# Kernel tuning notes

Measured on AMD Instinct MI355X. Metric: run time of the kernel, lower is better.

Reference implementation:

```python
import jax, jax.numpy as jnp
import numpy as np

B, L, LC, C, CTX, H = 4, 2048, 512, 1024, 1024, 16
D = C // H
EPS = 1e-6
SCALE = 1.0 / np.float32(np.sqrt(D))


def _ln(x):
    # LayerNorm32, elementwise_affine applied outside when present
    mu = jnp.mean(x, axis=-1, keepdims=True)
    var = jnp.var(x, axis=-1, keepdims=True)
    return (x - mu) * jax.lax.rsqrt(var + EPS)


def _attn(q, k, v):
    # q: [B,Lq,H,D], k/v: [B,Lk,H,D] -> [B,Lq,C]
    s = jnp.einsum('bqhd,bkhd->bhqk', q, k) * SCALE
    p = jax.nn.softmax(s, axis=-1)
    o = jnp.einsum('bhqk,bkhd->bqhd', p, v)
    return o.reshape(o.shape[0], o.shape[1], C)


def setup_inputs() -> dict:
    key = jax.random.key(0)
    ks = jax.random.split(key, 12)
    s = 0.02
    w = lambda k, shape: (jax.random.normal(k, shape, jnp.float32) * s)
    z = lambda n: jnp.zeros((n,), jnp.float32)
    return {
        'x': jax.random.normal(ks[0], (B, L, C), jnp.float32),
        'mod': jax.random.normal(ks[1], (B, C), jnp.float32),
        'context': jax.random.normal(ks[2], (B, LC, CTX), jnp.float32),
        'w_ada': w(ks[3], (C, 6 * C)), 'b_ada': z(6 * C),
        'w_qkv': w(ks[4], (C, 3 * C)), 'b_qkv': z(3 * C),
        'w_so': w(ks[5], (C, C)), 'b_so': z(C),
        'g_n2': jnp.ones((C,), jnp.float32), 'b_n2': z(C),
        'w_cq': w(ks[6], (C, C)), 'b_cq': z(C),
        'w_ckv': w(ks[7], (CTX, 2 * C)), 'b_ckv': z(2 * C),
        'w_co': w(ks[8], (C, C)), 'b_co': z(C),
        'w_m1': w(ks[9], (C, 4 * C)), 'b_m1': z(4 * C),
        'w_m2': w(ks[10], (4 * C, C)), 'b_m2': z(C),
    }


def reference(x, mod, context, w_ada, b_ada, w_qkv, b_qkv, w_so, b_so,
              g_n2, b_n2, w_cq, b_cq, w_ckv, b_ckv, w_co, b_co,
              w_m1, b_m1, w_m2, b_m2):
    # adaLN modulation: SiLU -> Linear(C, 6C) -> chunk(6)
    ada = jax.nn.silu(mod) @ w_ada + b_ada  # [B, 6C]
    sh_msa, sc_msa, g_msa, sh_mlp, sc_mlp, g_mlp = jnp.split(ada, 6, axis=-1)
    ex = lambda t: t[:, None, :]  # broadcast per-sample over its token run

    # --- MSA branch ---
    h = _ln(x) * (1.0 + ex(sc_msa)) + ex(sh_msa)
    qkv = (h @ w_qkv + b_qkv).reshape(B, L, 3, H, D)
    h = _attn(qkv[:, :, 0], qkv[:, :, 1], qkv[:, :, 2]) @ w_so + b_so
    x = x + h * ex(g_msa)

    # --- MCA branch (norm2 has affine) ---
    h = _ln(x) * g_n2 + b_n2
    q = (h @ w_cq + b_cq).reshape(B, L, H, D)
    kv = (context @ w_ckv + b_ckv).reshape(B, LC, 2, H, D)
    h = _attn(q, kv[:, :, 0], kv[:, :, 1]) @ w_co + b_co
    x = x + h

    # --- FFN branch ---
    h = _ln(x) * (1.0 + ex(sc_mlp)) + ex(sh_mlp)
    h = jax.nn.gelu(h @ w_m1 + b_m1, approximate=False) @ w_m2 + b_m2
    x = x + h * ex(g_mlp)
    return x
```

## Files before the change

### kernel.cpp

```cpp
#include <hip/hip_runtime.h>
#include <cstdint>

typedef __bf16 bf16;
typedef __bf16 bf16x8 __attribute__((ext_vector_type(8)));
typedef __bf16 bf16x4 __attribute__((ext_vector_type(4)));
typedef float  floatx4 __attribute__((ext_vector_type(4)));
typedef unsigned int uint32x4 __attribute__((ext_vector_type(4)));

#define B_  4
#define L_  2048
#define LC_ 512
#define C_  1024
#define H_  16
#define D_  64

typedef const __attribute__((address_space(1))) unsigned int* as1_u32p;
typedef __attribute__((address_space(3))) unsigned int* as3_u32p;

__device__ __forceinline__ void async16(const void* g, void* l) {
  __builtin_amdgcn_global_load_lds((as1_u32p)g, (as3_u32p)l, 16, 0, 0);
}

__device__ __forceinline__ floatx4 mfma16(bf16x8 a, bf16x8 b, floatx4 c) {
  return __builtin_amdgcn_mfma_f32_16x16x32_bf16(a, b, c, 0, 0, 0);
}

__device__ __forceinline__ bool dt_bf16(const unsigned* dt) { return dt[0] == 0x3F803F80u; }

__device__ __forceinline__ float rd(const void* p, size_t i, bool bf) {
  return bf ? (float)((const bf16*)p)[i] : ((const float*)p)[i];
}

__global__ __launch_bounds__(256) void k_cvt(const void* __restrict__ src, bf16* __restrict__ dst,
                                             int N, const unsigned* __restrict__ dt) {
  bool bf = dt_bf16(dt);
  int i = (blockIdx.x * 256 + threadIdx.x) * 4;
  if (i + 3 < N) {
    for (int j = 0; j < 4; ++j) dst[i + j] = (bf16)rd(src, i + j, bf);
  } else {
    for (int j = 0; j < 4 && i + j < N; ++j) dst[i + j] = (bf16)rd(src, i + j, bf);
  }
}

struct CvtSrcs { const void* s[9]; };
__global__ __launch_bounds__(256) void k_cvt_all(CvtSrcs c, bf16* __restrict__ dst,
                                                 const unsigned* __restrict__ dt) {
  bool bf = dt_bf16(dt);
  int i = blockIdx.x * 256 + threadIdx.x;
  if (i >= 15360) return;
  const int pre[10] = {0, 3072, 4096, 5120, 6144, 7168, 9216, 10240, 14336, 15360};
  int seg = 0;
  #pragma unroll
  for (int k = 1; k < 9; ++k) if (i >= pre[k]) seg = k;
  dst[i] = (bf16)rd(c.s[seg], i - pre[seg], bf);
}

__global__ __launch_bounds__(256) void k_silu(const void* __restrict__ mod, float* __restrict__ sm,
                                              const unsigned* __restrict__ dt) {
  bool bf = dt_bf16(dt);
  int i = blockIdx.x * 256 + threadIdx.x;
  if (i < B_ * C_) {
    float v = rd(mod, i, bf);
    sm[i] = v / (1.f + __expf(-v));
  }
}

__global__ __launch_bounds__(256) void k_ada(const float* __restrict__ sm, const void* __restrict__ w,
                                             float* __restrict__ part, const unsigned* __restrict__ dt) {
  bool bf = dt_bf16(dt);
  int idx = blockIdx.x * 256 + threadIdx.x;
  int b = idx / 6144, j = idx - b * 6144;
  int k0 = blockIdx.y * 256;
  const float* s = sm + b * C_;
  float acc = 0.f;
  if (bf) {
    const bf16* W = (const bf16*)w;
    for (int k = k0; k < k0 + 256; ++k) acc += s[k] * (float)W[(size_t)k * 6144 + j];
  } else {
    const float* W = (const float*)w;
    for (int k = k0; k < k0 + 256; ++k) acc += s[k] * W[(size_t)k * 6144 + j];
  }
  part[(size_t)blockIdx.y * 24576 + idx] = acc;
}

__global__ __launch_bounds__(256) void k_ada_red(const float* __restrict__ part, const void* __restrict__ bv,
                                                 float* __restrict__ ada, const unsigned* __restrict__ dt) {
  bool bf = dt_bf16(dt);
  int idx = blockIdx.x * 256 + threadIdx.x;
  int j = idx % 6144;
  ada[idx] = rd(bv, j, bf) + part[idx] + part[24576 + idx] + part[49152 + idx] + part[73728 + idx];
}

struct TransDesc { const void* src; bf16* dst; int R, Cc, nCb, pre; };
struct TransDescs { TransDesc d[7]; };
__global__ __launch_bounds__(256) void k_trans_all(TransDescs t, const unsigned* __restrict__ dt) {
  bool bf = dt_bf16(dt);
  __shared__ bf16 tile[32][33];
  int blk = blockIdx.x;
  int di = 0;
  #pragma unroll
  for (int i = 1; i < 7; ++i) if (blk >= t.d[i].pre) di = i;
  const void* src = t.d[di].src;
  bf16* dst = t.d[di].dst;
  int R = t.d[di].R, Cc = t.d[di].Cc;
  int local = blk - t.d[di].pre;
  int bx = local % t.d[di].nCb, by = local / t.d[di].nCb;
  int c0 = bx * 32, r0 = by * 32;
  int tx = threadIdx.x & 31, ty = threadIdx.x >> 5;
  for (int i = 0; i < 4; ++i)
    tile[ty * 4 + i][tx] = (bf16)rd(src, (size_t)(r0 + ty * 4 + i) * Cc + c0 + tx, bf);
  __syncthreads();
  for (int i = 0; i < 4; ++i)
    dst[(size_t)(c0 + ty * 4 + i) * R + r0 + tx] = tile[tx][ty * 4 + i];
}

__global__ __launch_bounds__(256) void k_vt(const bf16* __restrict__ src, int ld, int off, int Lk,
                                            bf16* __restrict__ VT) {
  __shared__ bf16 tile[32][33];
  int l0 = blockIdx.x * 32;
  int d0 = blockIdx.y * 32;
  int bh = blockIdx.z, b = bh >> 4, h = bh & 15;
  int tx = threadIdx.x & 31, ty = threadIdx.x >> 5;
  for (int i = 0; i < 4; ++i) {
    int l = l0 + ty * 4 + i;
    tile[ty * 4 + i][tx] = src[((size_t)b * Lk + l) * ld + off + h * 64 + d0 + tx];
  }
  __syncthreads();
  for (int i = 0; i < 4; ++i) {
    int d = d0 + ty * 4 + i;
    VT[((size_t)bh * 64 + d) * Lk + l0 + tx] = tile[tx][ty * 4 + i];
  }
}

__global__ __launch_bounds__(256) void k_ln(const void* __restrict__ xraw, const float* __restrict__ xf,
                                            const unsigned* __restrict__ dt, bf16* __restrict__ out,
                                            const float* __restrict__ ada, int scOff, int shOff, float scAdd,
                                            const bf16* __restrict__ gcol, const bf16* __restrict__ bcol) {
  int row = blockIdx.x;
  int b = row >> 11;
  int base = row * C_ + threadIdx.x * 4;
  float v[4];
  if (xf) {
    for (int i = 0; i < 4; ++i) v[i] = xf[base + i];
  } else {
    bool bf = dt_bf16(dt);
    for (int i = 0; i < 4; ++i) v[i] = rd(xraw, base + i, bf);
  }
  float s1 = 0.f, s2 = 0.f;
  for (int i = 0; i < 4; ++i) { s1 += v[i]; s2 += v[i] * v[i]; }
  for (int m = 1; m < 64; m <<= 1) { s1 += __shfl_xor(s1, m); s2 += __shfl_xor(s2, m); }
  __shared__ float r1[4], r2[4];
  int w = threadIdx.x >> 6;
  if ((threadIdx.x & 63) == 0) { r1[w] = s1; r2[w] = s2; }
  __syncthreads();
  s1 = r1[0] + r1[1] + r1[2] + r1[3];
  s2 = r2[0] + r2[1] + r2[2] + r2[3];
  float mu = s1 * (1.f / (float)C_);
  float var = fmaxf(s2 * (1.f / (float)C_) - mu * mu, 0.f);
  float rstd = rsqrtf(var + 1e-6f);
  for (int i = 0; i < 4; ++i) {
    int c = threadIdx.x * 4 + i;
    float sc, sh;
    if (ada) { sc = scAdd + ada[b * 6144 + scOff + c]; sh = ada[b * 6144 + shOff + c]; }
    else     { sc = (float)gcol[c];                    sh = (float)bcol[c]; }
    out[base + i] = (bf16)((v[i] - mu) * rstd * sc + sh);
  }
}

template <int MODE>
__global__ __launch_bounds__(256) void k_gemm(const bf16* __restrict__ A, const bf16* __restrict__ Bt,
                                              const bf16* __restrict__ bias, void* __restrict__ outv,
                                              int M, int N, int K,
                                              const void* __restrict__ resid,
                                              const float* __restrict__ ada, int gateOff,
                                              const unsigned* __restrict__ dt,
                                              float qs, int qN) {
  __shared__ bf16 As[2 * 8192];
  __shared__ bf16 Bs[2 * 8192];
  const int tid = threadIdx.x;
  const int w = tid >> 6, lane = tid & 63;
  const int wr = w & 1, wc = w >> 1;
  const int g = lane >> 4, t = lane & 15;

  const int nbx = gridDim.x;
  const int nwg = nbx * gridDim.y;
  const int orig = blockIdx.y * nbx + blockIdx.x;
  const int qq = nwg >> 3, rrm = nwg & 7;
  const int xcd = orig & 7, sidx = orig >> 3;
  const int wgid = (xcd < rrm ? xcd * (qq + 1) : rrm * (qq + 1) + (xcd - rrm) * qq) + sidx;
  const int rowA0 = (wgid / nbx) * 128, rowB0 = (wgid % nbx) * 128;

  const int scol = ((lane & 3) ^ ((lane >> 3) & 3)) * 8;
  const bf16* Ag = A  + (size_t)(rowA0 + w * 32 + (lane >> 2)) * K + scol;
  const bf16* Bg = Bt + (size_t)(rowB0 + w * 32 + (lane >> 2)) * K + scol;

  auto stage = [&](int kb, int bufsel) {
    bf16* Ad = As + bufsel * 8192 + w * 1024;
    bf16* Bd = Bs + bufsel * 8192 + w * 1024;
    async16(Ag + kb,                       Ad);
    async16(Ag + kb + (size_t)16 * K,      Ad + 512);
    async16(Ag + kb + 32,                  Ad + 4096);
    async16(Ag + kb + 32 + (size_t)16 * K, Ad + 4096 + 512);
    async16(Bg + kb,                       Bd);
    async16(Bg + kb + (size_t)16 * K,      Bd + 512);
    async16(Bg + kb + 32,                  Bd + 4096);
    async16(Bg + kb + 32 + (size_t)16 * K, Bd + 4096 + 512);
  };

  floatx4 acc[4][4];
  for (int i = 0; i < 4; ++i) for (int j = 0; j < 4; ++j) for (int r = 0; r < 4; ++r) acc[i][j][r] = 0.f;

  stage(0, 0);
  __syncthreads();

  const int rsw = (t >> 1) & 3;

  const int nkb = K >> 6;
  for (int it = 0; it < nkb; ++it) {
    const int cur = it & 1;
    if (it + 1 < nkb) stage((it + 1) << 6, cur ^ 1);
    const bf16* Asb = As + cur * 8192;
    const bf16* Bsb = Bs + cur * 8192;
    __builtin_amdgcn_s_setprio(1);
    #pragma unroll
    for (int kk = 0; kk < 2; ++kk) {
      const int gc = (g ^ rsw) * 8;
      bf16x8 af[4], bfr[4];
      #pragma unroll
      for (int mt = 0; mt < 4; ++mt) af[mt]  = *(const bf16x8*)&Asb[kk * 4096 + (wr * 64 + mt * 16 + t) * 32 + gc];
      #pragma unroll
      for (int nt = 0; nt < 4; ++nt) bfr[nt] = *(const bf16x8*)&Bsb[kk * 4096 + (wc * 64 + nt * 16 + t) * 32 + gc];
      #pragma unroll
      for (int mt = 0; mt < 4; ++mt)
        #pragma unroll
        for (int nt = 0; nt < 4; ++nt)
          acc[mt][nt] = mfma16(af[mt], bfr[nt], acc[mt][nt]);
    }
    __builtin_amdgcn_s_setprio(0);
    if (it + 1 < nkb) __syncthreads();
  }

  const bool bf = (MODE == 1 || MODE == 4) ? dt_bf16(dt) : false;
  for (int mt = 0; mt < 4; ++mt) {
    for (int nt = 0; nt < 4; ++nt) {
      int grow = rowA0 + wr * 64 + mt * 16 + g * 4;
      int gcol = rowB0 + wc * 64 + nt * 16 + t;
      float bvv = (float)bias[gcol];
      for (int r = 0; r < 4; ++r) {
        int rr = grow + r;
        float v = acc[mt][nt][r] + bvv;
        size_t idx = (size_t)rr * N + gcol;
        if (MODE == 0) {
          ((bf16*)outv)[idx] = (bf16)(v * ((gcol < qN) ? qs : 1.0f));
        } else if (MODE == 1) {
          float gt = ada[(rr >> 11) * 6144 + gateOff + gcol];
          ((float*)outv)[idx] = rd(resid, idx, bf) + v * gt;
        } else if (MODE == 2) {
          ((float*)outv)[idx] = ((const float*)resid)[idx] + v;
        } else if (MODE == 3) {
          ((bf16*)outv)[idx] = (bf16)(0.5f * v * (1.f + erff(v * 0.70710678118654752f)));
        } else {
          float gt = ada[(rr >> 11) * 6144 + gateOff + gcol];
          float val = ((const float*)resid)[idx] + v * gt;
          if (bf) ((bf16*)outv)[idx] = (bf16)val;
          else    ((float*)outv)[idx] = val;
        }
      }
    }
  }
}

__global__ __launch_bounds__(512) void k_attn(const bf16* __restrict__ Qb, int ldq, int qoff,
                                              const bf16* __restrict__ Kb, int ldk, int koff,
                                              const bf16* __restrict__ VT,
                                              bf16* __restrict__ Ob, int Lk) {
  __shared__ bf16 smem[24576];

  const int tid = threadIdx.x;
  const int w = tid >> 6, lane = tid & 63;
  const int g = lane >> 4, t = lane & 15;
  const int bh = blockIdx.y, b = bh >> 4, h = bh & 15;
  const int q0 = blockIdx.x * 128;

  const bf16* Q  = Qb + (size_t)(b * L_ + q0) * ldq + h * 64 + qoff;
  const bf16* K  = Kb + (size_t)b * Lk * ldk + h * 64 + koff;
  const bf16* Vt = VT + (size_t)bh * 64 * Lk;
  const int rowQ = w * 16 + t;
  bf16* O = Ob + ((size_t)(b * L_ + q0 + rowQ)) * C_ + h * 64;

  const int sp  = lane & 7;
  const int sq0 = w * 16 + (lane >> 3);
  const int sq1 = sq0 + 8;
  const int swq0 = (sp ^ (sq0 & 7)) * 8;
  const int swq1 = (sp ^ (sq1 & 7)) * 8;
  const int skr = w * 8 + (lane >> 3);
  const int swk = (sp ^ (skr & 7)) * 8;

  bf16* Ps  = smem;
  bf16* KB0 = smem + 8192;
  bf16* VB0 = smem + 16384;

  async16(Q + (size_t)sq0 * ldq + swq0, smem + w * 1024);
  async16(Q + (size_t)sq1 * ldq + swq1, smem + w * 1024 + 512);
  async16(K + (size_t)skr * ldk + swk, KB0 + w * 512);
  async16(Vt + (size_t)skr * Lk + swk, VB0 + w * 512);
  __syncthreads();

  bf16x8 bq[2];
  #pragma unroll
  for (int ko = 0; ko < 2; ++ko)
    bq[ko] = *(const bf16x8*)&smem[rowQ * 64 + (((ko * 4 + g) ^ (rowQ & 7)) * 8)];

  const int nt = Lk >> 6;

  if (nt > 1) {
    async16(K + (size_t)(64 + skr) * ldk + swk, KB0 + 4096 + w * 512);
  }

  floatx4 s[4];
  __builtin_amdgcn_s_setprio(1);
  #pragma unroll
  for (int mt = 0; mt < 4; ++mt) {
    floatx4 sa; for (int r = 0; r < 4; ++r) sa[r] = 0.f;
    #pragma unroll
    for (int ko = 0; ko < 2; ++ko) {
      int rowK = mt * 16 + t;
      bf16x8 ak = *(const bf16x8*)&KB0[rowK * 64 + (((ko * 4 + g) ^ (rowK & 7)) * 8)];
      sa = mfma16(ak, bq[ko], sa);
    }
    s[mt] = sa;
  }
  __builtin_amdgcn_s_setprio(0);
  __syncthreads();

  bf16x8 ones;
  #pragma unroll
  for (int i = 0; i < 8; ++i) ones[i] = (bf16)1.0f;

  floatx4 o_acc[4], o_sum;
  for (int d = 0; d < 4; ++d) for (int r = 0; r < 4; ++r) o_acc[d][r] = 0.f;
  for (int r = 0; r < 4; ++r) o_sum[r] = 0.f;

  const size_t kstep = (size_t)64 * ldk;
  const bf16* Kst = K + (size_t)(128 + skr) * ldk + swk;
  const bf16* Vst = Vt + (size_t)skr * Lk + 64 + swk;

  for (int ti = 0; ti < nt; ++ti) {
    const int cur = ti & 1;

    if (ti + 2 < nt) {
      async16(Kst, KB0 + cur * 4096 + w * 512);
    }
    if (ti + 1 < nt) {
      async16(Vst, VB0 + ((ti + 1) & 1) * 4096 + w * 512);
    }
    Kst += kstep; Vst += 64;

    float sv[16];
    #pragma unroll
    for (int mt = 0; mt < 4; ++mt)
      #pragma unroll
      for (int r = 0; r < 4; ++r) sv[mt * 4 + r] = exp2f(s[mt][r]);

    #pragma unroll
    for (int mt = 0; mt < 4; ++mt) {
      bf16x4 pk;
      for (int r = 0; r < 4; ++r) pk[r] = (bf16)sv[mt * 4 + r];
      int off = mt * 16 + g * 4;
      int chunk = off >> 3, sub = off & 7;
      *(bf16x4*)&Ps[rowQ * 64 + ((chunk ^ (rowQ & 7)) * 8) + sub] = pk;
    }

    if (ti + 1 < nt) {
      const bf16* Kc = KB0 + ((ti + 1) & 1) * 4096;
      __builtin_amdgcn_s_setprio(1);
      #pragma unroll
      for (int mt = 0; mt < 4; ++mt) {
        floatx4 sa; for (int r = 0; r < 4; ++r) sa[r] = 0.f;
        #pragma unroll
        for (int ko = 0; ko < 2; ++ko) {
          int rowK = mt * 16 + t;
          bf16x8 ak = *(const bf16x8*)&Kc[rowK * 64 + (((ko * 4 + g) ^ (rowK & 7)) * 8)];
          sa = mfma16(ak, bq[ko], sa);
        }
        s[mt] = sa;
      }
      __builtin_amdgcn_s_setprio(0);
    }

    const bf16* Vc = VB0 + cur * 4096;
    __builtin_amdgcn_s_setprio(1);
    #pragma unroll
    for (int ko = 0; ko < 2; ++ko) {
      bf16x8 bp = *(const bf16x8*)&Ps[rowQ * 64 + (((ko * 4 + g) ^ (rowQ & 7)) * 8)];
      o_sum = mfma16(ones, bp, o_sum);
      #pragma unroll
      for (int d = 0; d < 4; ++d) {
        int rowV = d * 16 + t;
        bf16x8 av = *(const bf16x8*)&Vc[rowV * 64 + (((ko * 4 + g) ^ (rowV & 7)) * 8)];
        o_acc[d] = mfma16(av, bp, o_acc[d]);
      }
    }
    __builtin_amdgcn_s_setprio(0);

    if (ti + 1 < nt) __syncthreads();
  }

  float rl = 1.f / o_sum[0];
  #pragma unroll
  for (int d = 0; d < 4; ++d) {
    bf16x4 ov;
    for (int r = 0; r < 4; ++r) ov[r] = (bf16)(o_acc[d][r] * rl);
    *(bf16x4*)&O[d * 16 + g * 4] = ov;
  }
}

extern "C" void kernel_launch(void* const* d_in, const int* in_sizes, int n_in,
                              void* d_out, int out_size, void* d_ws, size_t ws_size,
                              hipStream_t stream) {
  const void* x     = d_in[0];
  const void* mod   = d_in[1];
  const void* ctx   = d_in[2];
  const void* w_ada = d_in[3];
  const void* b_ada = d_in[4];
  const void* w_qkv = d_in[5];
  const void* b_qkv = d_in[6];
  const void* w_so  = d_in[7];
  const void* b_so  = d_in[8];
  const void* g_n2  = d_in[9];
  const void* b_n2  = d_in[10];
  const void* w_cq  = d_in[11];
  const void* b_cq  = d_in[12];
  const void* w_ckv = d_in[13];
  const void* b_ckv = d_in[14];
  const void* w_co  = d_in[15];
  const void* b_co  = d_in[16];
  const void* w_m1  = d_in[17];
  const void* b_m1  = d_in[18];
  const void* w_m2  = d_in[19];
  const void* b_m2  = d_in[20];
  const unsigned* dt = (const unsigned*)g_n2;

  char* p = (char*)d_ws;
  auto alloc = [&](size_t bytes) { char* r = p; p += (bytes + 255) & ~(size_t)255; return r; };
  float* sm    = (float*)alloc((size_t)B_ * C_ * 4);
  float* adp   = (float*)alloc((size_t)4 * 24576 * 4);
  float* ada   = (float*)alloc((size_t)B_ * 6144 * 4);
  bf16* wT_qkv = (bf16*)alloc((size_t)3072 * 1024 * 2);
  bf16* wT_so  = (bf16*)alloc((size_t)1024 * 1024 * 2);
  bf16* wT_cq  = (bf16*)alloc((size_t)1024 * 1024 * 2);
  bf16* wT_ckv = (bf16*)alloc((size_t)2048 * 1024 * 2);
  bf16* wT_co  = (bf16*)alloc((size_t)1024 * 1024 * 2);
  bf16* wT_m1  = (bf16*)alloc((size_t)4096 * 1024 * 2);
  bf16* wT_m2  = (bf16*)alloc((size_t)1024 * 4096 * 2);
  bf16* hb     = (bf16*)alloc((size_t)8192 * 1024 * 2);
  bf16* qkvb   = (bf16*)alloc((size_t)8192 * 3072 * 2);
  bf16* attn_o = (bf16*)alloc((size_t)8192 * 1024 * 2);
  float* xcur  = (float*)alloc((size_t)8192 * 1024 * 4);
  bf16* ctxb   = (bf16*)alloc((size_t)B_ * LC_ * 1024 * 2);
  bf16* biasb  = (bf16*)alloc(15360 * 2);
  bf16* bqkvb = biasb;
  bf16* bsob  = biasb + 3072;
  bf16* g2b   = biasb + 4096;
  bf16* b2b   = biasb + 5120;
  bf16* bcqb  = biasb + 6144;
  bf16* bckvb = biasb + 7168;
  bf16* bcob  = biasb + 9216;
  bf16* bm1b  = biasb + 10240;
  bf16* bm2b  = biasb + 14336;
  bf16* q2   = qkvb;
  bf16* kv   = qkvb + (size_t)8192 * 1024;
  bf16* gbuf = qkvb;
  bf16* vt   = hb;
  if (ws_size < (size_t)(p - (char*)d_ws)) return;

  dim3 blk(256);
  dim3 blkA(512);
  k_silu<<<16, blk, 0, stream>>>(mod, sm, dt);
  k_ada<<<dim3(96, 4), blk, 0, stream>>>(sm, w_ada, adp, dt);
  k_ada_red<<<96, blk, 0, stream>>>(adp, b_ada, ada, dt);
  k_cvt<<<2048, blk, 0, stream>>>(ctx, ctxb, B_ * LC_ * 1024, dt);
  CvtSrcs cs = {{b_qkv, b_so, g_n2, b_n2, b_cq, b_ckv, b_co, b_m1, b_m2}};
  k_cvt_all<<<60, blk, 0, stream>>>(cs, biasb, dt);
  TransDescs td = {{
    {w_qkv, wT_qkv, 1024, 3072,  96, 0},
    {w_so,  wT_so,  1024, 1024,  32, 3072},
    {w_cq,  wT_cq,  1024, 1024,  32, 4096},
    {w_ckv, wT_ckv, 1024, 2048,  64, 5120},
    {w_co,  wT_co,  1024, 1024,  32, 7168},
    {w_m1,  wT_m1,  1024, 4096, 128, 8192},
    {w_m2,  wT_m2,  4096, 1024,  32, 12288},
  }};
  k_trans_all<<<16384, blk, 0, stream>>>(td, dt);

  const float SC_L2E = 0.125f * 1.44269504088896f;

  k_ln<<<8192, blk, 0, stream>>>(x, nullptr, dt, hb, ada, 1024, 0, 1.0f, nullptr, nullptr);
  k_gemm<0><<<dim3(24, 64), blk, 0, stream>>>(hb, wT_qkv, bqkvb, qkvb, 8192, 3072, 1024, nullptr, nullptr, 0, dt, SC_L2E, 1024);
  k_vt<<<dim3(64, 2, 64), blk, 0, stream>>>(qkvb, 3072, 2048, L_, vt);
  k_attn<<<dim3(16, 64), blkA, 0, stream>>>(qkvb, 3072, 0, qkvb, 3072, 1024, vt, attn_o, L_);
  k_gemm<1><<<dim3(8, 64), blk, 0, stream>>>(attn_o, wT_so, bsob, xcur, 8192, 1024, 1024, x, ada, 2048, dt, 1.f, 0);

  k_ln<<<8192, blk, 0, stream>>>(nullptr, xcur, dt, hb, nullptr, 0, 0, 0.f, g2b, b2b);
  k_gemm<0><<<dim3(8, 64), blk, 0, stream>>>(hb, wT_cq, bcqb, q2, 8192, 1024, 1024, nullptr, nullptr, 0, dt, SC_L2E, 1024);
  k_gemm<0><<<dim3(16, 16), blk, 0, stream>>>(ctxb, wT_ckv, bckvb, kv, 2048, 2048, 1024, nullptr, nullptr, 0, dt, 1.f, 0);
  k_vt<<<dim3(16, 2, 64), blk, 0, stream>>>(kv, 2048, 1024, LC_, vt);
  k_attn<<<dim3(16, 64), blkA, 0, stream>>>(q2, 1024, 0, kv, 2048, 0, vt, attn_o, LC_);
  k_gemm<2><<<dim3(8, 64), blk, 0, stream>>>(attn_o, wT_co, bcob, xcur, 8192, 1024, 1024, xcur, nullptr, 0, dt, 1.f, 0);

  k_ln<<<8192, blk, 0, stream>>>(nullptr, xcur, dt, hb, ada, 4096, 3072, 1.0f, nullptr, nullptr);
  k_gemm<3><<<dim3(32, 64), blk, 0, stream>>>(hb, wT_m1, bm1b, gbuf, 8192, 4096, 1024, nullptr, nullptr, 0, dt, 1.f, 0);
  k_gemm<4><<<dim3(8, 64), blk, 0, stream>>>(gbuf, wT_m2, bm2b, d_out, 8192, 1024, 4096, xcur, ada, 5120, dt, 1.f, 0);
}
```

Before: 822.1 us.

## Add 256x256-tile 8-wave GEMM with XCD-aware remap for MLP up-projection

Adds a new GEMM kernel with 256x256 output tiles computed by 512 threads (8 waves, each 128x64). It double-buffers LDS, interleaves the async global-to-LDS loads with the MFMA phases, and remaps workgroup IDs across the 8 XCDs. Only the w_m1 GEMM with GELU uses it. The larger tile raises arithmetic intensity and cuts global and L2 traffic, at the cost of 128 KB of LDS and high register pressure, which limits occupancy to one block per CU.

```diff
diff --git a/kernel.cpp b/kernel.cpp
--- a/kernel.cpp
+++ b/kernel.cpp
@@ -249,6 +249,177 @@
       for (int r = 0; r < 4; ++r) {
         int rr = grow + r;
         float v = acc[mt][nt][r] + bvv;
+        size_t idx = (size_t)rr * N + gcol;
+        if (MODE == 0) {
+          ((bf16*)outv)[idx] = (bf16)(v * ((gcol < qN) ? qs : 1.0f));
+        } else if (MODE == 1) {
+          float gt = ada[(rr >> 11) * 6144 + gateOff + gcol];
+          ((float*)outv)[idx] = rd(resid, idx, bf) + v * gt;
+        } else if (MODE == 2) {
+          ((float*)outv)[idx] = ((const float*)resid)[idx] + v;
+        } else if (MODE == 3) {
+          ((bf16*)outv)[idx] = (bf16)(0.5f * v * (1.f + erff(v * 0.70710678118654752f)));
+        } else {
+          float gt = ada[(rr >> 11) * 6144 + gateOff + gcol];
+          float val = ((const float*)resid)[idx] + v * gt;
+          if (bf) ((bf16*)outv)[idx] = (bf16)val;
+          else    ((float*)outv)[idx] = val;
+        }
+      }
+    }
+  }
+}
+
+template <int MODE>
+__global__ __launch_bounds__(512) void k_gemm8(const bf16* __restrict__ A, const bf16* __restrict__ Bt,
+                                               const bf16* __restrict__ bias, void* __restrict__ outv,
+                                               int M, int N, int K,
+                                               const void* __restrict__ resid,
+                                               const float* __restrict__ ada, int gateOff,
+                                               const unsigned* __restrict__ dt,
+                                               float qs, int qN) {
+  __shared__ bf16 As[2 * 16384];
+  __shared__ bf16 Bs[2 * 16384];
+  const int tid = threadIdx.x;
+  const int lane = tid & 63;
+  const int wid = tid >> 6;
+  const int wrw = wid & 1, wcw = wid >> 1;
+  const int g = lane >> 4, t = lane & 15;
+
+  const int nbx = gridDim.x;
+  const int nwg = nbx * gridDim.y;
+  const int orig = blockIdx.y * nbx + blockIdx.x;
+  const int qq = nwg >> 3, rrm = nwg & 7;
+  const int xcd = orig & 7, sidx = orig >> 3;
+  const int wgid = (xcd < rrm ? xcd * (qq + 1) : rrm * (qq + 1) + (xcd - rrm) * qq) + sidx;
+  const int rowA0 = (wgid / nbx) * 256, rowB0 = (wgid % nbx) * 256;
+
+  const int srow = tid >> 3;
+  const int sch = ((tid & 7) ^ (srow & 7)) * 8;
+  const bf16* Ag = A  + (size_t)(rowA0 + srow) * K + sch;
+  const bf16* Bg = Bt + (size_t)(rowB0 + srow) * K + sch;
+  const size_t rstep = (size_t)64 * K;
+
+  floatx4 acc[8][4];
+  #pragma unroll
+  for (int i = 0; i < 8; ++i)
+    #pragma unroll
+    for (int j = 0; j < 4; ++j)
+      for (int r = 0; r < 4; ++r) acc[i][j][r] = 0.f;
+
+  const int nkb = K >> 6;
+  #pragma unroll
+  for (int j = 0; j < 4; ++j) async16(Ag + (size_t)j * rstep, As + j * 4096 + tid * 8);
+  #pragma unroll
+  for (int j = 0; j < 4; ++j) async16(Bg + (size_t)j * rstep, Bs + j * 4096 + tid * 8);
+
+  const int t7 = t & 7;
+
+  for (int T = 0; T < nkb; ++T) {
+    const int cur = T & 1;
+    const bool st = (T + 1 < nkb);
+    const int kb1 = (T + 1) << 6;
+    bf16* Asn = As + (cur ^ 1) * 16384;
+    bf16* Bsn = Bs + (cur ^ 1) * 16384;
+
+    if (st) {
+      async16(Ag + kb1,         Asn + tid * 8);
+      async16(Ag + rstep + kb1, Asn + 4096 + tid * 8);
+      asm volatile("s_waitcnt vmcnt(2)" ::: "memory");
+    } else {
+      asm volatile("s_waitcnt vmcnt(0)" ::: "memory");
+    }
+    __builtin_amdgcn_s_barrier();
+
+    const bf16* Ac = As + cur * 16384;
+    const bf16* Bc = Bs + cur * 16384;
+
+    bf16x8 bfr[4];
+    #pragma unroll
+    for (int nf = 0; nf < 4; ++nf)
+      bfr[nf] = *(const bf16x8*)&Bc[(wcw * 64 + nf * 16 + t) * 64 + ((0 * 4 + g) ^ t7) * 8];
+    {
+      bf16x8 af[4];
+      #pragma unroll
+      for (int mf = 0; mf < 4; ++mf)
+        af[mf] = *(const bf16x8*)&Ac[(wrw * 128 + mf * 16 + t) * 64 + ((0 * 4 + g) ^ t7) * 8];
+      __builtin_amdgcn_s_setprio(1);
+      #pragma unroll
+      for (int mf = 0; mf < 4; ++mf)
+        #pragma unroll
+        for (int nf = 0; nf < 4; ++nf)
+          acc[mf][nf] = mfma16(af[mf], bfr[nf], acc[mf][nf]);
+      __builtin_amdgcn_s_setprio(0);
+    }
+    if (st) {
+      async16(Ag + 2 * rstep + kb1, Asn + 2 * 4096 + tid * 8);
+      async16(Ag + 3 * rstep + kb1, Asn + 3 * 4096 + tid * 8);
+    }
+    {
+      bf16x8 af[4];
+      #pragma unroll
+      for (int mf = 0; mf < 4; ++mf)
+        af[mf] = *(const bf16x8*)&Ac[(wrw * 128 + (mf + 4) * 16 + t) * 64 + ((0 * 4 + g) ^ t7) * 8];
+      __builtin_amdgcn_s_setprio(1);
+      #pragma unroll
+      for (int mf = 0; mf < 4; ++mf)
+        #pragma unroll
+        for (int nf = 0; nf < 4; ++nf)
+          acc[mf + 4][nf] = mfma16(af[mf], bfr[nf], acc[mf + 4][nf]);
+      __builtin_amdgcn_s_setprio(0);
+    }
+    if (st) {
+      async16(Bg + kb1,         Bsn + tid * 8);
+      async16(Bg + rstep + kb1, Bsn + 4096 + tid * 8);
+    }
+    #pragma unroll
+    for (int nf = 0; nf < 4; ++nf)
+      bfr[nf] = *(const bf16x8*)&Bc[(wcw * 64 + nf * 16 + t) * 64 + ((1 * 4 + g) ^ t7) * 8];
+    {
+      bf16x8 af[4];
+      #pragma unroll
+      for (int mf = 0; mf < 4; ++mf)
+        af[mf] = *(const bf16x8*)&Ac[(wrw * 128 + mf * 16 + t) * 64 + ((1 * 4 + g) ^ t7) * 8];
+      __builtin_amdgcn_s_setprio(1);
+      #pragma unroll
+      for (int mf = 0; mf < 4; ++mf)
+        #pragma unroll
+        for (int nf = 0; nf < 4; ++nf)
+          acc[mf][nf] = mfma16(af[mf], bfr[nf], acc[mf][nf]);
+      __builtin_amdgcn_s_setprio(0);
+    }
+    if (st) {
+      async16(Bg + 2 * rstep + kb1, Bsn + 2 * 4096 + tid * 8);
+      async16(Bg + 3 * rstep + kb1, Bsn + 3 * 4096 + tid * 8);
+    }
+    {
+      bf16x8 af[4];
+      #pragma unroll
+      for (int mf = 0; mf < 4; ++mf)
+        af[mf] = *(const bf16x8*)&Ac[(wrw * 128 + (mf + 4) * 16 + t) * 64 + ((1 * 4 + g) ^ t7) * 8];
+      __builtin_amdgcn_s_setprio(1);
+      #pragma unroll
+      for (int mf = 0; mf < 4; ++mf)
+        #pragma unroll
+        for (int nf = 0; nf < 4; ++nf)
+          acc[mf + 4][nf] = mfma16(af[mf], bfr[nf], acc[mf + 4][nf]);
+      __builtin_amdgcn_s_setprio(0);
+    }
+    asm volatile("s_waitcnt lgkmcnt(0)" ::: "memory");
+    __builtin_amdgcn_s_barrier();
+  }
+
+  const bool bf = (MODE == 1 || MODE == 4) ? dt_bf16(dt) : false;
+  #pragma unroll
+  for (int mf = 0; mf < 8; ++mf) {
+    #pragma unroll
+    for (int nf = 0; nf < 4; ++nf) {
+      int grow = rowA0 + wrw * 128 + mf * 16 + g * 4;
+      int gcol = rowB0 + wcw * 64 + nf * 16 + t;
+      float bvv = (float)bias[gcol];
+      for (int r = 0; r < 4; ++r) {
+        int rr = grow + r;
+        float v = acc[mf][nf][r] + bvv;
         size_t idx = (size_t)rr * N + gcol;
         if (MODE == 0) {
           ((bf16*)outv)[idx] = (bf16)(v * ((gcol < qN) ? qs : 1.0f));
@@ -509,6 +680,6 @@
   k_gemm<2><<<dim3(8, 64), blk, 0, stream>>>(attn_o, wT_co, bcob, xcur, 8192, 1024, 1024, xcur, nullptr, 0, dt, 1.f, 0);
 
   k_ln<<<8192, blk, 0, stream>>>(nullptr, xcur, dt, hb, ada, 4096, 3072, 1.0f, nullptr, nullptr);
-  k_gemm<3><<<dim3(32, 64), blk, 0, stream>>>(hb, wT_m1, bm1b, gbuf, 8192, 4096, 1024, nullptr, nullptr, 0, dt, 1.f, 0);
+  k_gemm8<3><<<dim3(16, 32), blkA, 0, stream>>>(hb, wT_m1, bm1b, gbuf, 8192, 4096, 1024, nullptr, nullptr, 0, dt, 1.f, 0);
   k_gemm<4><<<dim3(8, 64), blk, 0, stream>>>(gbuf, wT_m2, bm2b, d_out, 8192, 1024, 4096, xcur, ada, 5120, dt, 1.f, 0);
 }
```

Measured after the change: 815.7 us. About the same (-0.8%).
